# Kernel tuning notes

Measured on AMD Instinct MI355X. Metric: run time of the kernel, lower is better.

## Reference

```python
import jax, jax.numpy as jnp
import numpy as np

B, C_IN, C_OUT, H, W = 64, 1024, 1024, 16, 16
HEADS, C_RED = 8, 512  # reduced_ch = 1024 // 2
N = H * W
EPS = 1e-5  # BatchNorm eps (eval mode, running stats)
NEG_SLOPE = 0.2  # PyG GATConv default leaky_relu slope


def build_grid_edge_index(P, Pw):
    # 4-neighbor grid + one self-loop per node, directed [2, E]
    edges = []
    for i in range(P):
        for j in range(Pw):
            u = i * Pw + j
            if i - 1 >= 0: edges.append([u, u - Pw])
            if i + 1 < P:  edges.append([u, u + Pw])
            if j - 1 >= 0: edges.append([u, u - 1])
            if j + 1 < Pw: edges.append([u, u + 1])
            edges.append([u, u])
    return jnp.asarray(np.array(edges, dtype=np.int32).T)


def setup_inputs() -> dict:
    key = jax.random.key(0)
    ks = jax.random.split(key, 10)
    x = jax.random.normal(ks[0], (B, C_IN, H, W), jnp.float32)
    w_reduce = jax.random.normal(ks[1], (C_RED, C_IN), jnp.float32) * 0.02
    g_red = jnp.ones((C_RED,), jnp.float32); b_red = jnp.zeros((C_RED,), jnp.float32)
    m_red = jax.random.normal(ks[2], (C_RED,), jnp.float32) * 0.1
    v_red = jax.random.uniform(ks[3], (C_RED,), jnp.float32) + 0.5
    w_gat = jax.random.normal(ks[4], (C_RED, HEADS * C_RED), jnp.float32) * 0.02
    att_src = jax.random.normal(ks[5], (HEADS, C_RED), jnp.float32) * 0.1
    att_dst = jax.random.normal(ks[6], (HEADS, C_RED), jnp.float32) * 0.1
    gat_bias = jnp.zeros((C_RED,), jnp.float32)
    w_restore = jax.random.normal(ks[7], (C_OUT, C_RED), jnp.float32) * 0.02
    g_res = jnp.ones((C_OUT,), jnp.float32); b_res = jnp.zeros((C_OUT,), jnp.float32)
    m_res = jax.random.normal(ks[8], (C_OUT,), jnp.float32) * 0.1
    v_res = jax.random.uniform(ks[9], (C_OUT,), jnp.float32) + 0.5
    edge_index = build_grid_edge_index(H, W)
    return dict(x=x, w_reduce=w_reduce, g_red=g_red, b_red=b_red, m_red=m_red, v_red=v_red,
                w_gat=w_gat, att_src=att_src, att_dst=att_dst, gat_bias=gat_bias,
                w_restore=w_restore, g_res=g_res, b_res=b_res, m_res=m_res, v_res=v_res,
                edge_index=edge_index)


def _bn(x, g, b, m, v):  # channel-last, eval mode
    return (x - m) * (g * jax.lax.rsqrt(v + EPS)) + b


def reference(x, w_reduce, g_red, b_red, m_red, v_red, w_gat, att_src, att_dst,
              gat_bias, w_restore, g_res, b_res, m_res, v_res, edge_index):
    xh = jnp.transpose(x, (0, 2, 3, 1))                 # [B,H,W,C_in] NHWC
    res = xh                                            # identity residual (C_in == C_out)
    xr = jax.nn.relu(_bn(xh @ w_reduce.T, g_red, b_red, m_red, v_red))  # [B,H,W,C_red]
    nodes = xr.reshape(B, N, C_RED)                     # per-sample grid graph nodes

    # --- GATConv (heads=HEADS, concat=False), batched over B ---
    xp = (nodes @ w_gat).reshape(B, N, HEADS, C_RED)    # projected per-head features
    a_src = jnp.einsum('bnhc,hc->bnh', xp, att_src)
    a_dst = jnp.einsum('bnhc,hc->bnh', xp, att_dst)
    src, dst = edge_index[0], edge_index[1]
    logits = jax.nn.leaky_relu(a_src[:, src] + a_dst[:, dst], NEG_SLOPE)  # [B,E,HEADS]
    seg_max = jax.vmap(lambda a: jax.ops.segment_max(a, dst, num_segments=N))(logits)
    e = jnp.exp(logits - seg_max[:, dst])
    seg_sum = jax.vmap(lambda a: jax.ops.segment_sum(a, dst, num_segments=N))(e)
    alpha = e / seg_sum[:, dst]                          # softmax over incoming edges
    msg = alpha[..., None] * xp[:, src]                  # [B,E,HEADS,C_red]
    agg = jax.vmap(lambda m_: jax.ops.segment_sum(m_, dst, num_segments=N))(msg)
    gat_out = agg.mean(axis=2) + gat_bias                # concat=False -> head mean, [B,N,C_red]

    out = gat_out.reshape(B, H, W, C_RED) @ w_restore.T  # 1x1 restore conv
    out = _bn(out, g_res, b_res, m_res, v_res)
    out = jax.nn.relu(out + res)
    return jnp.transpose(out, (0, 3, 1, 2))              # [B,C_out,H,W]
```

## Files before the change

### kernel.cpp

```cpp
#include <hip/hip_runtime.h>


typedef unsigned short u16;
typedef __attribute__((ext_vector_type(4))) unsigned short u16x4;
typedef __attribute__((ext_vector_type(8))) unsigned short u16x8;
typedef __attribute__((ext_vector_type(8))) __bf16 bf16x8;
typedef __attribute__((ext_vector_type(2))) __bf16 bf16x2;
typedef __attribute__((ext_vector_type(4))) float f32x4;

#if defined(__has_builtin)
#if __has_builtin(__builtin_amdgcn_fdot2_f32_bf16)
#define HAVE_DOT2 1
#endif
#endif

#define B_    64
#define CIN   1024
#define CRED  512
#define COUT  1024
#define NPIX  256
#define HEADS 8
#define KGAT  4096
#define MTOT  16384
#define EPSB  1e-5f

__device__ __forceinline__ float b2f(u16 u) {
  union { unsigned u; float f; } c; c.u = ((unsigned)u) << 16; return c.f;
}
__device__ __forceinline__ u16 f2b(float f) {
  union { float f; unsigned u; } c; c.f = f;
  unsigned r = (c.u + 0x7FFFu + ((c.u >> 16) & 1u)) >> 16;
  return (u16)r;
}

__device__ __forceinline__ void gload_lds16(const void* g, void* lds) {
  __builtin_amdgcn_global_load_lds(
      (const __attribute__((address_space(1))) void*)g,
      (__attribute__((address_space(3))) void*)lds, 16, 0, 0);
}

union U8u {
  u16x8 v;
  bf16x2 p[4];
};

__global__ __launch_bounds__(256) void alphapre_kernel(
    const float* __restrict__ a_all, u16* __restrict__ alf_g)
{
  const int nh = blockIdx.x * 256 + threadIdx.x;
  const int ng = nh >> 3, h = nh & 7;
  const int n = ng & 255;
  const size_t nbase = (size_t)(ng >> 8) * NPIX;
  const int gi = n >> 4, gj = n & 15;
  int vv[5];
  vv[0] = n;
  vv[1] = (gi > 0)  ? n - 16 : -1;
  vv[2] = (gi < 15) ? n + 16 : -1;
  vv[3] = (gj > 0)  ? n - 1  : -1;
  vv[4] = (gj < 15) ? n + 1  : -1;
  const float* a_src = a_all;
  const float* a_dst = a_all + (size_t)MTOT * HEADS;
  const float ad = a_dst[(nbase + n) * HEADS + h];
  float l[5]; float mx = -1e30f;
#pragma unroll
  for (int e = 0; e < 5; ++e) {
    if (vv[e] >= 0) {
      const float xx = a_src[(nbase + vv[e]) * HEADS + h] + ad;
      l[e] = xx > 0.f ? xx : 0.2f * xx;
      mx = fmaxf(mx, l[e]);
    } else l[e] = -1e30f;
  }
  float s = 0.f, ee[5];
#pragma unroll
  for (int e = 0; e < 5; ++e) {
    ee[e] = (vv[e] >= 0) ? __expf(l[e] - mx) : 0.f;
    s += ee[e];
  }
  const float inv = 0.125f / s;
#pragma unroll
  for (int e = 0; e < 5; ++e)
    alf_g[(size_t)ng * 40 + e * 8 + h] = f2b(ee[e] * inv);
}

__global__ __launch_bounds__(512, 4) void gemmf2_kernel(
    const u16* __restrict__ A, const u16* __restrict__ Btp,
    const u16* __restrict__ alf_g, const float* __restrict__ gat_bias,
    u16* __restrict__ gat)
{
  extern __shared__ u16 lds[];
  u16* Ys = lds;

  const int tid = threadIdx.x;
  const int wave = tid >> 6, lane = tid & 63;
  const int wm = wave >> 1, wn = wave & 1;
  const int l15 = lane & 15, l4 = lane >> 4;

  const int raw = blockIdx.x;
  const int lin = (raw & 7) * 256 + (raw >> 3);
  const int img = lin >> 5;
  const int ntile = lin & 31;
  const int n0 = ntile * 128;
  const int jbg = ntile * 16;
  const size_t nbase = (size_t)img * NPIX;

  int offA[2], dstA[2];
#pragma unroll
  for (int i = 0; i < 2; ++i) {
    const int f = i * 512 + tid;
    const int r = f >> 2;
    const int kb = (f & 3) ^ ((r >> 1) & 3);
    offA[i] = r * 512 + kb * 8;
    dstA[i] = (i * 512 + wave * 64) * 8;
  }
  const int rB = tid >> 2;
  const int kbB = (tid & 3) ^ ((rB >> 1) & 3);
  const int offB = rB * 512 + kbB * 8;
  const int dstB = wave * 64 * 8;

  const u16* gA = A + (size_t)img * 256 * 512;
  const u16* gB = Btp + (size_t)n0 * 512;

  auto stage = [&](int t) {
    const int d = (t & 1) * 12288;
    gload_lds16(gA + t * 32 + offA[0], &lds[d + dstA[0]]);
    gload_lds16(gA + t * 32 + offA[1], &lds[d + dstA[1]]);
    gload_lds16(gB + t * 32 + offB, &lds[d + 8192 + dstB]);
  };

  f32x4 acc[4][4];
#pragma unroll
  for (int i = 0; i < 4; ++i)
#pragma unroll
    for (int j = 0; j < 4; ++j) acc[i][j] = f32x4{0.f, 0.f, 0.f, 0.f};

  const int kq = (l4 ^ ((l15 >> 1) & 3)) * 8;
  const int aBase = (wm * 64 + l15) * 32 + kq;
  const int bBase = 8192 + (wn * 64 + l15) * 32 + kq;

  stage(0);

  for (int t = 0; t < 16; ++t) {
    asm volatile("s_waitcnt vmcnt(0)" ::: "memory");
    __builtin_amdgcn_s_barrier();
    const int d = (t & 1) * 12288;
    bf16x8 af[4], bfr[4];
#pragma unroll
    for (int f = 0; f < 4; ++f) {
      af[f]  = *(const bf16x8*)&lds[d + aBase + f * 512];
      bfr[f] = *(const bf16x8*)&lds[d + bBase + f * 512];
    }
    if (t < 15) stage(t + 1);
    __builtin_amdgcn_s_setprio(1);
#pragma unroll
    for (int fm = 0; fm < 4; ++fm)
#pragma unroll
      for (int fn = 0; fn < 4; ++fn)
        acc[fm][fn] = __builtin_amdgcn_mfma_f32_16x16x32_bf16(
            bfr[fn], af[fm], acc[fm][fn], 0, 0, 0);
    __builtin_amdgcn_s_setprio(0);
  }
  __syncthreads();

#pragma unroll
  for (int fm = 0; fm < 4; ++fm) {
    const int nloc = wm * 64 + fm * 16 + l15;
#pragma unroll
    for (int fn = 0; fn < 4; ++fn) {
      const int cloc = wn * 64 + fn * 16 + l4 * 4;
      u16x4 ov;
#pragma unroll
      for (int r = 0; r < 4; ++r) ov[r] = f2b(acc[fm][fn][r]);
      *(u16x4*)&Ys[nloc * 136 + cloc] = ov;
    }
  }
  __syncthreads();

  const int n = tid >> 1, half = tid & 1;
  const int gi = n >> 4, gj = n & 15;
  int vv[5];
  vv[0] = n;
  vv[1] = (gi > 0)  ? n - 16 : n;
  vv[2] = (gi < 15) ? n + 16 : n;
  vv[3] = (gj > 0)  ? n - 1  : n;
  vv[4] = (gj < 15) ? n + 1  : n;
  U8u au[5];
  {
    const u16* ag = alf_g + (nbase + n) * 40;
#pragma unroll
    for (int e = 0; e < 5; ++e) au[e].v = *(const u16x8*)&ag[e * 8];
  }
  float o[8];
  {
    const int jb = jbg + half * 8;
    const float4 b0 = *(const float4*)&gat_bias[jb];
    const float4 b1 = *(const float4*)&gat_bias[jb + 4];
    o[0] = b0.x; o[1] = b0.y; o[2] = b0.z; o[3] = b0.w;
    o[4] = b1.x; o[5] = b1.y; o[6] = b1.z; o[7] = b1.w;
  }
#pragma unroll
  for (int e = 0; e < 5; ++e) {
    const u16* yrow = &Ys[vv[e] * 136 + half * 64];
#if defined(HAVE_DOT2)
#pragma unroll
    for (int k = 0; k < 8; ++k) {
      U8u yu;
      yu.v = *(const u16x8*)&yrow[k * 8];
      float s = o[k];
      s = __builtin_amdgcn_fdot2_f32_bf16(yu.p[0], au[e].p[0], s, false);
      s = __builtin_amdgcn_fdot2_f32_bf16(yu.p[1], au[e].p[1], s, false);
      s = __builtin_amdgcn_fdot2_f32_bf16(yu.p[2], au[e].p[2], s, false);
      s = __builtin_amdgcn_fdot2_f32_bf16(yu.p[3], au[e].p[3], s, false);
      o[k] = s;
    }
#else
    float a8[8];
#pragma unroll
    for (int h = 0; h < 8; ++h) a8[h] = b2f(au[e].v[h]);
#pragma unroll
    for (int k = 0; k < 8; ++k) {
      const u16x8 yv = *(const u16x8*)&yrow[k * 8];
#pragma unroll
      for (int h = 0; h < 8; ++h) o[k] += a8[h] * b2f(yv[h]);
    }
#endif
  }
  u16x8 ov;
#pragma unroll
  for (int k = 0; k < 8; ++k) ov[k] = f2b(o[k]);
  *(u16x8*)&gat[(nbase + n) * (size_t)CRED + jbg + half * 8] = ov;
}

__global__ __launch_bounds__(512, 1) void gemm_res2_kernel(
    const u16* __restrict__ A, const u16* __restrict__ Bt,
    float* __restrict__ out32,
    const float* __restrict__ pg, const float* __restrict__ pb,
    const float* __restrict__ pm, const float* __restrict__ pv,
    const float* __restrict__ auxf)
{
  extern __shared__ u16 lds[];
  const int tid = threadIdx.x;
  const int wave = tid >> 6, lane = tid & 63;
  const int wm = wave >> 2, wn = wave & 3;
  const int l15 = lane & 15, l4 = lane >> 4;

  int lin = blockIdx.y * 4 + blockIdx.x;
  lin = (lin & 7) * 32 + (lin >> 3);
  const int m0 = (lin >> 2) * 256;
  const int n0 = (lin & 3) * 256;

  int offS[2], ldsS[2];
#pragma unroll
  for (int i = 0; i < 2; ++i) {
    const int f = i * 512 + tid;
    const int r = f >> 2;
    const int kb = (f & 3) ^ ((r >> 1) & 3);
    offS[i] = r * 512 + kb * 8;
    ldsS[i] = (i * 512 + wave * 64) * 8;
  }
  const u16* gA = A + (size_t)m0 * 512;
  const u16* gB = Bt + (size_t)n0 * 512;

  auto stageA = [&](int kt) {
    const int bo = (kt & 3) * 16384;
    gload_lds16(gA + kt * 32 + offS[0], &lds[bo + ldsS[0]]);
    gload_lds16(gA + kt * 32 + offS[1], &lds[bo + ldsS[1]]);
  };
  auto stageB = [&](int kt) {
    const int bo = (kt & 3) * 16384 + 8192;
    gload_lds16(gB + kt * 32 + offS[0], &lds[bo + ldsS[0]]);
    gload_lds16(gB + kt * 32 + offS[1], &lds[bo + ldsS[1]]);
  };

  f32x4 acc[8][4];
#pragma unroll
  for (int i = 0; i < 8; ++i)
#pragma unroll
    for (int j = 0; j < 4; ++j) acc[i][j] = f32x4{0.f, 0.f, 0.f, 0.f};

  const int kq = (l4 ^ ((l15 >> 1) & 3)) * 8;
  const int aBase = (wm * 128 + l15) * 32 + kq;
  const int bBase = 8192 + (wn * 64 + l15) * 32 + kq;

  stageA(0); stageB(0); stageA(1); stageB(1);

  for (int kt = 0; kt < 16; ++kt) {
    if (kt == 15) { asm volatile("s_waitcnt vmcnt(0)" ::: "memory"); }
    else         { asm volatile("s_waitcnt vmcnt(4)" ::: "memory"); }
    __builtin_amdgcn_s_barrier();
    const int bo = (kt & 3) * 16384;
    bf16x8 bfr[4], af0[4], af1[4];
#pragma unroll
    for (int f = 0; f < 4; ++f)
      bfr[f] = *(const bf16x8*)&lds[bo + bBase + f * 512];
#pragma unroll
    for (int f = 0; f < 4; ++f)
      af0[f] = *(const bf16x8*)&lds[bo + aBase + f * 512];
#pragma unroll
    for (int f = 0; f < 4; ++f)
      af1[f] = *(const bf16x8*)&lds[bo + aBase + (f + 4) * 512];
    if (kt < 14) { stageA(kt + 2); stageB(kt + 2); }
    __builtin_amdgcn_s_setprio(1);
#pragma unroll
    for (int fm = 0; fm < 4; ++fm)
#pragma unroll
      for (int fn = 0; fn < 4; ++fn)
        acc[fm][fn] = __builtin_amdgcn_mfma_f32_16x16x32_bf16(
            af0[fm], bfr[fn], acc[fm][fn], 0, 0, 0);
#pragma unroll
    for (int fm = 0; fm < 4; ++fm)
#pragma unroll
      for (int fn = 0; fn < 4; ++fn)
        acc[fm + 4][fn] = __builtin_amdgcn_mfma_f32_16x16x32_bf16(
            af1[fm], bfr[fn], acc[fm + 4][fn], 0, 0, 0);
    __builtin_amdgcn_s_setprio(0);
  }

  const int rowb = m0 + wm * 128 + l4 * 4;
#pragma unroll
  for (int fn = 0; fn < 4; ++fn) {
    const int col = n0 + wn * 64 + fn * 16 + l15;
    const float sc = pg[col] * rsqrtf(pv[col] + EPSB);
    const float off = pb[col] - pm[col] * sc;
#pragma unroll
    for (int fm = 0; fm < 8; ++fm) {
      const int row = rowb + fm * 16;
      const int bimg = row >> 8, p0 = row & 255;
      const size_t oa = (size_t)bimg * (COUT * NPIX) + (size_t)col * NPIX + p0;
      const float4 rv = *(const float4*)&auxf[oa];
      float4 ov;
      ov.x = fmaxf(acc[fm][fn][0] * sc + off + rv.x, 0.f);
      ov.y = fmaxf(acc[fm][fn][1] * sc + off + rv.y, 0.f);
      ov.z = fmaxf(acc[fm][fn][2] * sc + off + rv.z, 0.f);
      ov.w = fmaxf(acc[fm][fn][3] * sc + off + rv.w, 0.f);
      *(float4*)&out32[oa] = ov;
    }
  }
}

__global__ __launch_bounds__(256) void wgatp_kernel(
    const float* __restrict__ w_gat, u16* __restrict__ out)
{
  __shared__ float tile[64][65];
  const int cb = blockIdx.x;
  const int kb = blockIdx.y;
  const int t = threadIdx.x;
  const int jl = t & 7, h = (t >> 3) & 7, k4 = t >> 6;
#pragma unroll
  for (int i = 0; i < 16; ++i) {
    const int kl = k4 * 16 + i;
    tile[kl][jl * 8 + h] =
        w_gat[(size_t)(kb * 64 + kl) * KGAT + h * 512 + cb * 8 + jl];
  }
  __syncthreads();
#pragma unroll
  for (int i = 0; i < 4; ++i) {
    const int idx = i * 256 + t;
    const int cl = idx >> 4;
    const int kq = (idx & 15) * 4;
    u16x4 ov;
#pragma unroll
    for (int q = 0; q < 4; ++q) ov[q] = f2b(tile[kq + q][cl]);
    *(u16x4*)&out[(size_t)(cb * 64 + cl) * CRED + kb * 64 + kq] = ov;
  }
}

__global__ __launch_bounds__(256, 2) void gemm_redf_kernel(
    const float* __restrict__ x, const u16* __restrict__ Bt,
    u16* __restrict__ out16,
    const float* __restrict__ pg, const float* __restrict__ pb,
    const float* __restrict__ pm, const float* __restrict__ pv)
{
  __shared__ u16 As[64 * 32];
  __shared__ u16 Bs[128 * 32];
  const int tid = threadIdx.x;
  const int wave = tid >> 6, lane = tid & 63;
  const int gx = gridDim.x;
  const int nwg = gx * gridDim.y;
  int lin = blockIdx.y * gx + blockIdx.x;
  lin = (lin & 7) * (nwg >> 3) + (lin >> 3);
  const int m0 = (lin / gx) * 64, n0 = (lin % gx) * 128;
  const int bimg = m0 >> 8, p0 = m0 & 255;

  const float* xsrc = x + (size_t)bimg * CIN * NPIX + p0 + lane;

  int offB[2], dstB[2];
#pragma unroll
  for (int i = 0; i < 2; ++i) {
    const int f = i * 256 + tid;
    const int r = f >> 2;
    const int kb = (f & 3) ^ ((r >> 1) & 3);
    offB[i] = r * CIN + kb * 8;
    dstB[i] = (i * 256 + wave * 64) * 8;
  }
  const u16* gB = Bt + (size_t)n0 * CIN;

  const int aWr = (lane * 4 + (wave ^ ((lane >> 1) & 3))) * 8;

  f32x4 acc[2][4];
#pragma unroll
  for (int i = 0; i < 2; ++i)
#pragma unroll
    for (int j = 0; j < 4; ++j) acc[i][j] = f32x4{0.f, 0.f, 0.f, 0.f};

  const int wr = wave >> 1, wc = wave & 1;
  const int l15 = lane & 15, l4 = lane >> 4;
  const int kq = (l4 ^ ((l15 >> 1) & 3)) * 8;

  float av[8];
#pragma unroll
  for (int j = 0; j < 8; ++j) av[j] = xsrc[(wave * 8 + j) * NPIX];

  for (int kt = 0; kt < CIN; kt += 32) {
    u16x8 pvv;
#pragma unroll
    for (int j = 0; j < 8; ++j) pvv[j] = f2b(av[j]);
    *(u16x8*)&As[aWr] = pvv;
    gload_lds16(gB + kt + offB[0], &Bs[dstB[0]]);
    gload_lds16(gB + kt + offB[1], &Bs[dstB[1]]);
    __syncthreads();
    if (kt + 32 < CIN) {
#pragma unroll
      for (int j = 0; j < 8; ++j)
        av[j] = xsrc[(kt + 32 + wave * 8 + j) * NPIX];
    }
    bf16x8 af[2], bfr[4];
#pragma unroll
    for (int f = 0; f < 2; ++f)
      af[f] = *(const bf16x8*)&As[(wr * 32 + f * 16 + l15) * 32 + kq];
#pragma unroll
    for (int f = 0; f < 4; ++f)
      bfr[f] = *(const bf16x8*)&Bs[(wc * 64 + f * 16 + l15) * 32 + kq];
#pragma unroll
    for (int fm = 0; fm < 2; ++fm)
#pragma unroll
      for (int fn = 0; fn < 4; ++fn)
        acc[fm][fn] = __builtin_amdgcn_mfma_f32_16x16x32_bf16(
            af[fm], bfr[fn], acc[fm][fn], 0, 0, 0);
    __syncthreads();
  }

  const int rowb = m0 + wr * 32 + (lane >> 4) * 4;
#pragma unroll
  for (int fn = 0; fn < 4; ++fn) {
    const int col = n0 + wc * 64 + fn * 16 + l15;
    const float sc = pg[col] * rsqrtf(pv[col] + EPSB);
    const float off = pb[col] - pm[col] * sc;
#pragma unroll
    for (int fm = 0; fm < 2; ++fm) {
      const int row = rowb + fm * 16;
#pragma unroll
      for (int r = 0; r < 4; ++r) {
        const float y = fmaxf(acc[fm][fn][r] * sc + off, 0.f);
        out16[(size_t)(row + r) * CRED + col] = f2b(y);
      }
    }
  }
}

__global__ __launch_bounds__(256) void cvt2_kernel(
    const float* __restrict__ s0, u16* __restrict__ d0,
    const float* __restrict__ s1, u16* __restrict__ d1, int half)
{
  const int bi = blockIdx.x;
  const float* src = (bi < half) ? s0 : s1;
  u16* dst = (bi < half) ? d0 : d1;
  const int i = ((bi < half ? bi : bi - half) * 256 + threadIdx.x) * 8;
  const float4 a = *(const float4*)&src[i];
  const float4 b = *(const float4*)&src[i + 4];
  u16x8 o;
  o[0] = f2b(a.x); o[1] = f2b(a.y); o[2] = f2b(a.z); o[3] = f2b(a.w);
  o[4] = f2b(b.x); o[5] = f2b(b.y); o[6] = f2b(b.z); o[7] = f2b(b.w);
  *(u16x8*)&dst[i] = o;
}

__global__ __launch_bounds__(128) void attproj_kernel(
    const float* __restrict__ w_gat, const float* __restrict__ att_src,
    const float* __restrict__ att_dst, float* __restrict__ P)
{
  __shared__ float av[CRED];
  const int bi = blockIdx.x;
  const int sh = bi & 15, q = bi >> 4;
  const int s = sh >> 3, h = sh & 7;
  const float* att = (s == 0) ? att_src : att_dst;
  for (int t = threadIdx.x; t < CRED; t += 128) av[t] = att[h * CRED + t];
  __syncthreads();
  const int c = q * 128 + threadIdx.x;
  const float* wrow = w_gat + (size_t)c * KGAT + h * CRED;
  float acc = 0.f;
  for (int j = 0; j < CRED; j += 4) {
    const float4 w = *(const float4*)&wrow[j];
    acc += w.x * av[j] + w.y * av[j + 1] + w.z * av[j + 2] + w.w * av[j + 3];
  }
  P[(size_t)sh * CRED + c] = acc;
}

__global__ __launch_bounds__(256) void att_kernel(
    const u16* __restrict__ xr, const float* __restrict__ P,
    float* __restrict__ a_all)
{
  const int wave = threadIdx.x >> 6, lane = threadIdx.x & 63;
  const int m = blockIdx.x * 4 + wave;
  const int sh = lane & 15, q = lane >> 4;
  const u16* xp = xr + (size_t)m * CRED + q * 128;
  const float* Pp = P + (size_t)sh * CRED + q * 128;
  float s = 0.f;
#pragma unroll
  for (int c = 0; c < 128; c += 8) {
    u16x8 xv = *(const u16x8*)&xp[c];
#pragma unroll
    for (int t = 0; t < 8; ++t) s += b2f(xv[t]) * Pp[c + t];
  }
  s += __shfl_xor(s, 16);
  s += __shfl_xor(s, 32);
  if (q == 0)
    a_all[(size_t)(sh >> 3) * MTOT * HEADS + (size_t)m * HEADS + (sh & 7)] = s;
}

extern "C" void kernel_launch(void* const* d_in, const int* in_sizes, int n_in,
                              void* d_out, int out_size, void* d_ws, size_t ws_size,
                              hipStream_t stream)
{
  const float* x         = (const float*)d_in[0];
  const float* w_reduce  = (const float*)d_in[1];
  const float* g_red     = (const float*)d_in[2];
  const float* b_red     = (const float*)d_in[3];
  const float* m_red     = (const float*)d_in[4];
  const float* v_red     = (const float*)d_in[5];
  const float* w_gat     = (const float*)d_in[6];
  const float* att_src   = (const float*)d_in[7];
  const float* att_dst   = (const float*)d_in[8];
  const float* gat_bias  = (const float*)d_in[9];
  const float* w_restore = (const float*)d_in[10];
  const float* g_res     = (const float*)d_in[11];
  const float* b_res     = (const float*)d_in[12];
  const float* m_res     = (const float*)d_in[13];
  const float* v_res     = (const float*)d_in[14];

  constexpr size_t SZ_XR   = (size_t)MTOT * CRED * 2;
  constexpr size_t SZ_GAT  = SZ_XR;
  constexpr size_t SZ_WGT  = (size_t)KGAT * CRED * 2;
  constexpr size_t SZ_WRD  = (size_t)CRED * CIN * 2;
  constexpr size_t SZ_WRS  = (size_t)COUT * CRED * 2;
  constexpr size_t SZ_P    = (size_t)16 * CRED * 4;
  constexpr size_t SZ_AALL = (size_t)2 * MTOT * HEADS * 4;
  char* ws = (char*)d_ws;
  u16*   xr     = (u16*)ws;
  u16*   gat    = (u16*)(ws + SZ_XR);
  u16*   WgT2p  = (u16*)(ws + SZ_XR + SZ_GAT);
  u16*   wred_b = (u16*)(ws + SZ_XR + SZ_GAT + SZ_WGT);
  u16*   wres_b = (u16*)(ws + SZ_XR + SZ_GAT + SZ_WGT + SZ_WRD);
  float* P      = (float*)(ws + SZ_XR + SZ_GAT + SZ_WGT + SZ_WRD + SZ_WRS);
  float* a_all  = (float*)(ws + SZ_XR + SZ_GAT + SZ_WGT + SZ_WRD + SZ_WRS + SZ_P);
  u16*   alf_g  = (u16*)(ws + SZ_XR + SZ_GAT + SZ_WGT + SZ_WRD + SZ_WRS + SZ_P + SZ_AALL);
  float* outp   = (float*)d_out;

  hipFuncSetAttribute((const void*)gemmf2_kernel,
                      hipFuncAttributeMaxDynamicSharedMemorySize, 69632);
  hipFuncSetAttribute((const void*)gemm_res2_kernel,
                      hipFuncAttributeMaxDynamicSharedMemorySize, 131072);

  wgatp_kernel<<<dim3(64, 8), 256, 0, stream>>>(w_gat, WgT2p);
  cvt2_kernel<<<512, 256, 0, stream>>>(
      w_reduce, wred_b, w_restore, wres_b, 256);
  gemm_redf_kernel<<<dim3(4, 256), 256, 0, stream>>>(
      x, wred_b, xr, g_red, b_red, m_red, v_red);
  attproj_kernel<<<64, 128, 0, stream>>>(w_gat, att_src, att_dst, P);
  att_kernel<<<MTOT / 4, 256, 0, stream>>>(xr, P, a_all);
  alphapre_kernel<<<512, 256, 0, stream>>>(a_all, alf_g);
  gemmf2_kernel<<<2048, 512, 69632, stream>>>(
      xr, WgT2p, alf_g, gat_bias, gat);
  gemm_res2_kernel<<<dim3(4, 64), 512, 131072, stream>>>(
      gat, wres_b, outp, g_res, b_res, m_res, v_res, x);
  (void)in_sizes; (void)n_in; (void)out_size; (void)ws_size;
}
```

Before: 236.4 us.

## Shrink restore GEMM tile to 256x128 with double buffering for higher occupancy

Restructures the restore-conv GEMM from 256x256 tiles with a 4-deep LDS ring to 256x128 tiles with a 2-stage double buffer. Each wave now holds 4x4 accumulators instead of 8x4, and LDS use drops to 48KB, so launch bounds allow up to 4 blocks per CU. The grid grows to 512 blocks, which gives better CU coverage on the final GEMM and epilogue. In exchange, the prefetch is only one stage deep and waits on vmcnt(0) every iteration, and B-operand reuse per block is lower.

```diff
diff --git a/kernel.cpp b/kernel.cpp
--- a/kernel.cpp
+++ b/kernel.cpp
@@ -230,7 +230,7 @@
   *(u16x8*)&gat[(nbase + n) * (size_t)CRED + jbg + half * 8] = ov;
 }
 
-__global__ __launch_bounds__(512, 1) void gemm_res2_kernel(
+__global__ __launch_bounds__(512, 4) void gemm_res3_kernel(
     const u16* __restrict__ A, const u16* __restrict__ Bt,
     float* __restrict__ out32,
     const float* __restrict__ pg, const float* __restrict__ pb,
@@ -240,89 +240,79 @@
   extern __shared__ u16 lds[];
   const int tid = threadIdx.x;
   const int wave = tid >> 6, lane = tid & 63;
-  const int wm = wave >> 2, wn = wave & 3;
+  const int wm = wave >> 1, wn = wave & 1;
   const int l15 = lane & 15, l4 = lane >> 4;
 
-  int lin = blockIdx.y * 4 + blockIdx.x;
-  lin = (lin & 7) * 32 + (lin >> 3);
-  const int m0 = (lin >> 2) * 256;
-  const int n0 = (lin & 3) * 256;
-
-  int offS[2], ldsS[2];
+  const int raw = blockIdx.x;
+  const int lin = (raw & 7) * 64 + (raw >> 3);
+  const int m0 = (lin >> 3) * 256;
+  const int n0 = (lin & 7) * 128;
+
+  int offA[2], dstA[2];
 #pragma unroll
   for (int i = 0; i < 2; ++i) {
     const int f = i * 512 + tid;
     const int r = f >> 2;
     const int kb = (f & 3) ^ ((r >> 1) & 3);
-    offS[i] = r * 512 + kb * 8;
-    ldsS[i] = (i * 512 + wave * 64) * 8;
-  }
+    offA[i] = r * 512 + kb * 8;
+    dstA[i] = (i * 512 + wave * 64) * 8;
+  }
+  const int rB = tid >> 2;
+  const int kbB = (tid & 3) ^ ((rB >> 1) & 3);
+  const int offB = rB * 512 + kbB * 8;
+  const int dstB = wave * 64 * 8;
+
   const u16* gA = A + (size_t)m0 * 512;
   const u16* gB = Bt + (size_t)n0 * 512;
 
-  auto stageA = [&](int kt) {
-    const int bo = (kt & 3) * 16384;
-    gload_lds16(gA + kt * 32 + offS[0], &lds[bo + ldsS[0]]);
-    gload_lds16(gA + kt * 32 + offS[1], &lds[bo + ldsS[1]]);
+  auto stage = [&](int t) {
+    const int d = (t & 1) * 12288;
+    gload_lds16(gA + t * 32 + offA[0], &lds[d + dstA[0]]);
+    gload_lds16(gA + t * 32 + offA[1], &lds[d + dstA[1]]);
+    gload_lds16(gB + t * 32 + offB, &lds[d + 8192 + dstB]);
   };
-  auto stageB = [&](int kt) {
-    const int bo = (kt & 3) * 16384 + 8192;
-    gload_lds16(gB + kt * 32 + offS[0], &lds[bo + ldsS[0]]);
-    gload_lds16(gB + kt * 32 + offS[1], &lds[bo + ldsS[1]]);
-  };
-
-  f32x4 acc[8][4];
-#pragma unroll
-  for (int i = 0; i < 8; ++i)
+
+  f32x4 acc[4][4];
+#pragma unroll
+  for (int i = 0; i < 4; ++i)
 #pragma unroll
     for (int j = 0; j < 4; ++j) acc[i][j] = f32x4{0.f, 0.f, 0.f, 0.f};
 
   const int kq = (l4 ^ ((l15 >> 1) & 3)) * 8;
-  const int aBase = (wm * 128 + l15) * 32 + kq;
+  const int aBase = (wm * 64 + l15) * 32 + kq;
   const int bBase = 8192 + (wn * 64 + l15) * 32 + kq;
 
-  stageA(0); stageB(0); stageA(1); stageB(1);
-
-  for (int kt = 0; kt < 16; ++kt) {
-    if (kt == 15) { asm volatile("s_waitcnt vmcnt(0)" ::: "memory"); }
-    else         { asm volatile("s_waitcnt vmcnt(4)" ::: "memory"); }
+  stage(0);
+
+  for (int t = 0; t < 16; ++t) {
+    asm volatile("s_waitcnt vmcnt(0)" ::: "memory");
     __builtin_amdgcn_s_barrier();
-    const int bo = (kt & 3) * 16384;
-    bf16x8 bfr[4], af0[4], af1[4];
-#pragma unroll
-    for (int f = 0; f < 4; ++f)
-      bfr[f] = *(const bf16x8*)&lds[bo + bBase + f * 512];
-#pragma unroll
-    for (int f = 0; f < 4; ++f)
-      af0[f] = *(const bf16x8*)&lds[bo + aBase + f * 512];
-#pragma unroll
-    for (int f = 0; f < 4; ++f)
-      af1[f] = *(const bf16x8*)&lds[bo + aBase + (f + 4) * 512];
-    if (kt < 14) { stageA(kt + 2); stageB(kt + 2); }
+    const int d = (t & 1) * 12288;
+    bf16x8 af[4], bfr[4];
+#pragma unroll
+    for (int f = 0; f < 4; ++f) {
+      af[f]  = *(const bf16x8*)&lds[d + aBase + f * 512];
+      bfr[f] = *(const bf16x8*)&lds[d + bBase + f * 512];
+    }
+    if (t < 15) stage(t + 1);
     __builtin_amdgcn_s_setprio(1);
 #pragma unroll
     for (int fm = 0; fm < 4; ++fm)
 #pragma unroll
       for (int fn = 0; fn < 4; ++fn)
         acc[fm][fn] = __builtin_amdgcn_mfma_f32_16x16x32_bf16(
-            af0[fm], bfr[fn], acc[fm][fn], 0, 0, 0);
-#pragma unroll
-    for (int fm = 0; fm < 4; ++fm)
-#pragma unroll
-      for (int fn = 0; fn < 4; ++fn)
-        acc[fm + 4][fn] = __builtin_amdgcn_mfma_f32_16x16x32_bf16(
-            af1[fm], bfr[fn], acc[fm + 4][fn], 0, 0, 0);
+            af[fm], bfr[fn], acc[fm][fn], 0, 0, 0);
     __builtin_amdgcn_s_setprio(0);
   }
 
-  const int rowb = m0 + wm * 128 + l4 * 4;
+  const int rowb = m0 + wm * 64 + l4 * 4;
 #pragma unroll
   for (int fn = 0; fn < 4; ++fn) {
     const int col = n0 + wn * 64 + fn * 16 + l15;
     const float sc = pg[col] * rsqrtf(pv[col] + EPSB);
     const float off = pb[col] - pm[col] * sc;
 #pragma unroll
-    for (int fm = 0; fm < 8; ++fm) {
+    for (int fm = 0; fm < 4; ++fm) {
       const int row = rowb + fm * 16;
       const int bimg = row >> 8, p0 = row & 255;
       const size_t oa = (size_t)bimg * (COUT * NPIX) + (size_t)col * NPIX + p0;
@@ -556,8 +546,8 @@
 
   hipFuncSetAttribute((const void*)gemmf2_kernel,
                       hipFuncAttributeMaxDynamicSharedMemorySize, 69632);
-  hipFuncSetAttribute((const void*)gemm_res2_kernel,
-                      hipFuncAttributeMaxDynamicSharedMemorySize, 131072);
+  hipFuncSetAttribute((const void*)gemm_res3_kernel,
+                      hipFuncAttributeMaxDynamicSharedMemorySize, 49152);
 
   wgatp_kernel<<<dim3(64, 8), 256, 0, stream>>>(w_gat, WgT2p);
   cvt2_kernel<<<512, 256, 0, stream>>>(
@@ -569,7 +559,7 @@
   alphapre_kernel<<<512, 256, 0, stream>>>(a_all, alf_g);
   gemmf2_kernel<<<2048, 512, 69632, stream>>>(
       xr, WgT2p, alf_g, gat_bias, gat);
-  gemm_res2_kernel<<<dim3(4, 64), 512, 131072, stream>>>(
+  gemm_res3_kernel<<<512, 512, 49152, stream>>>(
       gat, wres_b, outp, g_res, b_res, m_res, v_res, x);
   (void)in_sizes; (void)n_in; (void)out_size; (void)ws_size;
 }
```

After: 234.7 us. No clear change (-0.7%).
